# Kernel tuning notes

Hardware: AMD Instinct MI355X
Metric: run time of the kernel (lower is better)

## Reference

```python
import jax, jax.numpy as jnp
from jax import lax
import numpy as np
import math

# ---- static hyperparameters (from init_kwargs) ----
NUM_RAY = 64
NUM_RAY2 = NUM_RAY * NUM_RAY
NUM_SAMPLE = 64
STEP = 1.0 / (NUM_SAMPLE - 1)
RK = 3                       # RK4Range: neighbor cube side
K = 64                       # Num_RIGuassKernel per axis
PH = (192, 192, 192)         # PhantomSize (D, H, W)
THETA_X, THETA_Y, THETA_Z = 0.1, 0.05, 0.02
CENTER = (0.5, 0.5, 0.5)

# ---- constant neighbor offsets and kernel-center grids (Process_Parameter) ----
half = (RK - 1) // 2
_r = np.arange(-half, half + 1)
Xr_np, Yr_np, Zr_np = np.meshgrid(_r, _r, _r)
XR = jnp.asarray(Xr_np.flatten().reshape(1, RK ** 3), dtype=jnp.float32)
YR = jnp.asarray(Yr_np.flatten().reshape(1, RK ** 3), dtype=jnp.float32)
ZR = jnp.asarray(Zr_np.flatten().reshape(1, RK ** 3), dtype=jnp.float32)
_c = np.linspace(0, 1, K, dtype='float32')
Xc_np, Yc_np, Zc_np = np.meshgrid(_c, _c, _c)
XC = jnp.asarray(Xc_np.flatten())
YC = jnp.asarray(Yc_np.flatten())
ZC = jnp.asarray(Zc_np.flatten())

# ---- rotation matrices (Theta2TransMatrix) ----
def _build_transmats():
    def ry(t):
        c, s = math.cos(t), math.sin(t)
        return np.array([[1, 0, 0, 0], [0, c, -s, 0], [0, s, c, 0], [0, 0, 0, 1]], dtype=np.float64)
    def rx(t):
        c, s = math.cos(t), math.sin(t)
        return np.array([[c, 0, -s, 0], [0, 1, 0, 0], [s, 0, c, 0], [0, 0, 0, 1]], dtype=np.float64)
    def rz(t):
        c, s = math.cos(t), math.sin(t)
        return np.array([[c, -s, 0, 0], [s, c, 0, 0], [0, 0, 1, 0], [0, 0, 0, 1]], dtype=np.float64)
    RY, RY_ = ry(-THETA_Y), ry(THETA_Y)
    RX, RX_ = rx(THETA_X), rx(-THETA_X)
    RZ, RZ_ = rz(-THETA_Z), rz(THETA_Z)
    cx, cy, cz = CENTER
    S1 = np.eye(4); S1[3, :3] = [-cx, -cy, -cz]
    S2 = np.eye(4); S2[3, :3] = [cx, cy, cz]
    M_crd = S1 @ RZ @ RY @ RX @ S2
    M_drv = RX_ @ RY_ @ RZ_
    return jnp.asarray(M_crd, dtype=jnp.float32), jnp.asarray(M_drv, dtype=jnp.float32)

M_CRD, M_DRV = _build_transmats()


def _indexdist(x, y, z, RI):
    # x,y,z: [N]; RI: [K^3, 2] -> Gaussian-kernel interpolated n and spatial derivatives
    X, Y, Z = x[:, None], y[:, None], z[:, None]
    Xn = jnp.clip(jnp.round(X * K) + XR, 0.0, K - 1.0)
    Yn = jnp.clip(jnp.round(Y * K) + YR, 0.0, K - 1.0)
    Zn = jnp.clip(jnp.round(Z * K) + ZR, 0.0, K - 1.0)
    lin = (K * K * Yn + K * Xn + Zn).astype(jnp.int32)   # [N, RK^3]
    dx = XC[lin] - X
    dy = YC[lin] - Y
    dz = ZC[lin] - Z
    A = RI[lin, 0]
    sig = RI[lin, 1]
    inv_s2 = 1.0 / (sig * sig)
    ni = jnp.exp(-(dx * dx + dy * dy + dz * dz) * 0.5 * inv_s2) + 2e-7
    norm = jnp.sum(ni, axis=1)
    nu = ni * A
    nx = jnp.sum(nu * dx * inv_s2, axis=1)
    ny = jnp.sum(nu * dy * inv_s2, axis=1)
    nz = jnp.sum(nu * dz * inv_s2, axis=1)
    ndx = jnp.sum(ni * dx * inv_s2, axis=1)
    ndy = jnp.sum(ni * dy * inv_s2, axis=1)
    ndz = jnp.sum(ni * dz * inv_s2, axis=1)
    nu_s = jnp.sum(nu, axis=1)
    n = nu_s / norm
    inv_norm2 = 1.0 / (norm * norm)
    nx = (norm * nx - nu_s * ndx) * inv_norm2
    ny = (norm * ny - nu_s * ndy) * inv_norm2
    nz = (norm * nz - nu_s * ndz) * inv_norm2
    return n, nx, ny, nz


def _rayeq(z0, xy0, RI):
    ones = jnp.ones_like(z0)
    t = jnp.stack([xy0[:, 2], xy0[:, 0], z0, ones], axis=1) @ M_CRD
    n, dndx_, dndy_, dndz_ = _indexdist(t[:, 1], t[:, 0], t[:, 2], RI)
    d = jnp.stack([dndy_, dndx_, dndz_, ones], axis=1) @ M_DRV
    dndx, dndz, dndy = d[:, 1], d[:, 2], d[:, 0]
    dX1 = xy0[:, 1]
    dX2 = (dndx - dndz * dX1) * (1.0 + dX1 * dX1) / n
    dY1 = xy0[:, 3]
    dY2 = (dndy - dndz * dY1) * (1.0 + dY1 * dY1) / n
    return jnp.stack([dX1, dX2, dY1, dY2], axis=1)


def _ray_tracing(xyz0, RI):
    def step_fn(xyz, _):
        deriv = _rayeq(xyz[:, 4], xyz[:, 0:4], RI)
        xyzi = jnp.concatenate([xyz[:, 0:4] + deriv * STEP, (xyz[:, 4] + STEP)[:, None]], axis=1)
        return xyzi, xyzi
    _, rest = lax.scan(step_fn, xyz0, None, length=NUM_SAMPLE - 1)
    return jnp.concatenate([xyz0[None], rest], axis=0)   # [S, N, 5]


def _resize_axis_linear(a, axis, out_len):
    # align_corners=True 1D linear resize along `axis`
    in_len = a.shape[axis]
    pos = jnp.linspace(0.0, in_len - 1.0, out_len)
    i0 = jnp.clip(jnp.floor(pos).astype(jnp.int32), 0, in_len - 2)
    w = (pos - i0.astype(pos.dtype)).astype(a.dtype)
    a0 = jnp.take(a, i0, axis=axis)
    a1 = jnp.take(a, i0 + 1, axis=axis)
    shape = [1] * a.ndim
    shape[axis] = out_len
    w = w.reshape(shape)
    return a0 * (1.0 - w) + a1 * w


def _grid_sample_3d(vol, gx, gy, gz):
    # torch F.grid_sample trilinear, align_corners=True, padding_mode='zeros'
    D, H, W = vol.shape
    ix = (gx + 1.0) * 0.5 * (W - 1)
    iy = (gy + 1.0) * 0.5 * (H - 1)
    iz = (gz + 1.0) * 0.5 * (D - 1)
    x0 = jnp.floor(ix); y0 = jnp.floor(iy); z0 = jnp.floor(iz)
    fx = ix - x0; fy = iy - y0; fz = iz - z0
    out = jnp.zeros_like(ix)
    for dz in (0, 1):
        for dyy in (0, 1):
            for dxx in (0, 1):
                xi = x0 + dxx; yi = y0 + dyy; zi = z0 + dz
                wgt = (jnp.where(dxx == 1, fx, 1.0 - fx)
                       * jnp.where(dyy == 1, fy, 1.0 - fy)
                       * jnp.where(dz == 1, fz, 1.0 - fz))
                inb = ((xi >= 0) & (xi <= W - 1) & (yi >= 0) & (yi <= H - 1)
                       & (zi >= 0) & (zi <= D - 1))
                xc = jnp.clip(xi, 0, W - 1).astype(jnp.int32)
                yc = jnp.clip(yi, 0, H - 1).astype(jnp.int32)
                zc = jnp.clip(zi, 0, D - 1).astype(jnp.int32)
                out = out + jnp.where(inb, wgt * vol[zc, yc, xc], 0.0)
    return out


def setup_inputs() -> dict:
    key = jax.random.key(0)
    k1, k2, k3, k4, k5 = jax.random.split(key, 5)
    Phantom = jax.random.uniform(k1, (1, 1) + PH, dtype=jnp.float32)
    A = jax.random.uniform(k2, (K ** 3, 1), dtype=jnp.float32) * 0.9 + 0.1
    sig = jax.random.uniform(k3, (K ** 3, 1), dtype=jnp.float32) * 0.8 + 0.2
    RefractionIndex = jnp.concatenate([A, sig], axis=1)
    xy = jax.random.uniform(k4, (NUM_RAY2, 2), dtype=jnp.float32) * 0.8 + 0.1
    slopes = jax.random.normal(k5, (NUM_RAY2, 2), dtype=jnp.float32) * 0.05
    z0 = jnp.zeros((NUM_RAY2, 1), dtype=jnp.float32)
    # layout [x, dx/dz, y, dy/dz, z]
    RayInit = jnp.concatenate([xy[:, :1], slopes[:, :1], xy[:, 1:], slopes[:, 1:], z0], axis=1)
    return {"Phantom": Phantom, "RefractionIndex": RefractionIndex, "RayInit": RayInit}


def reference(Phantom, RefractionIndex, RayInit):
    RayInit = RayInit.reshape(NUM_RAY2, 5)
    RI = RefractionIndex.reshape(K ** 3, 2)
    paths = _ray_tracing(RayInit, RI)          # [S, N, 5]
    paths = paths * 2.0 - 1.0
    # paths -> [3, R, R, S] mesh of (x, y, z) coordinates
    mesh = jnp.stack([
        paths[:, :, 0].T.reshape(NUM_RAY, NUM_RAY, NUM_SAMPLE),
        paths[:, :, 2].T.reshape(NUM_RAY, NUM_RAY, NUM_SAMPLE),
        paths[:, :, 4].T.reshape(NUM_RAY, NUM_RAY, NUM_SAMPLE),
    ], axis=0)
    # trilinear resize (align_corners=True) to PhantomSize
    for ax, out_len in zip((1, 2, 3), PH):
        mesh = _resize_axis_linear(mesh, ax, out_len)   # [3, D, H, W]
    vol = Phantom.reshape(PH)
    out = _grid_sample_3d(vol, mesh[0], mesh[1], mesh[2])
    return out.reshape((1, 1) + PH)
```

## Files before the change

kernel.cpp:

```cpp
#include <hip/hip_runtime.h>
#include <math.h>

#define NRAY2 4096
#define NSAMP 64
#define PHD 192
#define PLANE (PHD*PHD)
constexpr float STEP = 1.0f / 63.0f;

struct Mats { float crd[16]; float drv[16]; };

static void mat_mul4(const double* A, const double* B, double* C) {
    for (int i = 0; i < 4; ++i)
        for (int j = 0; j < 4; ++j) {
            double s = 0.0;
            for (int k = 0; k < 4; ++k) s += A[i*4+k] * B[k*4+j];
            C[i*4+j] = s;
        }
}

static void build_mats(Mats& M) {
    const double tx = 0.1, ty = 0.05, tz = 0.02;
    const double cx = 0.5, cy = 0.5, cz = 0.5;
    auto ry = [](double t, double* m) {
        double c = cos(t), s = sin(t);
        double v[16] = {1,0,0,0, 0,c,-s,0, 0,s,c,0, 0,0,0,1};
        for (int i = 0; i < 16; ++i) m[i] = v[i];
    };
    auto rx = [](double t, double* m) {
        double c = cos(t), s = sin(t);
        double v[16] = {c,0,-s,0, 0,1,0,0, s,0,c,0, 0,0,0,1};
        for (int i = 0; i < 16; ++i) m[i] = v[i];
    };
    auto rz = [](double t, double* m) {
        double c = cos(t), s = sin(t);
        double v[16] = {c,-s,0,0, s,c,0,0, 0,0,1,0, 0,0,0,1};
        for (int i = 0; i < 16; ++i) m[i] = v[i];
    };
    double RY[16], RY_[16], RX[16], RX_[16], RZ[16], RZ_[16];
    ry(-ty, RY); ry(ty, RY_);
    rx(tx, RX);  rx(-tx, RX_);
    rz(-tz, RZ); rz(tz, RZ_);
    double S1[16] = {1,0,0,0, 0,1,0,0, 0,0,1,0, -cx,-cy,-cz,1};
    double S2[16] = {1,0,0,0, 0,1,0,0, 0,0,1,0,  cx, cy, cz,1};
    double t1[16], t2[16], t3[16], Mc[16], Md[16];
    mat_mul4(S1, RZ, t1);
    mat_mul4(t1, RY, t2);
    mat_mul4(t2, RX, t3);
    mat_mul4(t3, S2, Mc);
    mat_mul4(RX_, RY_, t1);
    mat_mul4(t1, RZ_, Md);
    for (int i = 0; i < 16; ++i) { M.crd[i] = (float)Mc[i]; M.drv[i] = (float)Md[i]; }
}

template<int CTRL>
__device__ __forceinline__ void dpp_level8(float* v) {
    int t[8];
    #pragma unroll
    for (int i = 0; i < 8; ++i)
        t[i] = __builtin_amdgcn_update_dpp(0, __float_as_int(v[i]), CTRL, 0xF, 0xF, true);
    #pragma unroll
    for (int i = 0; i < 8; ++i) v[i] += __int_as_float(t[i]);
}

__device__ __forceinline__ void red8_16(float* v) {
    dpp_level8<0x121>(v);
    dpp_level8<0x122>(v);
    dpp_level8<0x124>(v);
    dpp_level8<0x128>(v);
}

__global__ __launch_bounds__(64, 1) void ray_trace_kernel(
    const float* __restrict__ RI,
    const float* __restrict__ RayInit,
    float* __restrict__ meshXT,
    float* __restrict__ meshYT,
    Mats M)
{
    __shared__ float lX[NSAMP][4];
    __shared__ float lY[NSAMP][4];

    const int tid = threadIdx.x;
    const int nb  = tid & 15;
    const int rl  = tid >> 4;
    const int ray = blockIdx.x * 4 + rl;
    const bool act2 = nb < 11;

    const int n1 = nb, n2 = nb + 16;
    const float xr1 = (float)((n1/3)%3 - 1), yr1 = (float)(n1/9 - 1), zr1 = (float)(n1%3 - 1);
    const float xr2 = (float)((n2/3)%3 - 1), yr2 = (float)(n2/9 - 1), zr2 = (float)(n2%3 - 1);

    float X  = RayInit[ray*5 + 0];
    float dX = RayInit[ray*5 + 1];
    float Y  = RayInit[ray*5 + 2];
    float dY = RayInit[ray*5 + 3];
    float z  = RayInit[ray*5 + 4];

    if (nb == 0) { lX[0][rl] = X*2.0f - 1.0f; lY[0][rl] = Y*2.0f - 1.0f; }

    auto prep = [&](float pX, float pY, float pz,
                    float& ox, float& oy, float& oz,
                    float& X1, float& Y1, float& Z1,
                    float& X2, float& Y2, float& Z2,
                    float2& r1, float2& r2) {
        float x  = pY*M.crd[1] + pX*M.crd[5] + pz*M.crd[9]  + M.crd[13];
        float y  = pY*M.crd[0] + pX*M.crd[4] + pz*M.crd[8]  + M.crd[12];
        float zz = pY*M.crd[2] + pX*M.crd[6] + pz*M.crd[10] + M.crd[14];
        float rx_ = rintf(x*64.0f), ry_ = rintf(y*64.0f), rz_ = rintf(zz*64.0f);
        X1 = __builtin_amdgcn_fmed3f(rx_ + xr1, 0.0f, 63.0f);
        Y1 = __builtin_amdgcn_fmed3f(ry_ + yr1, 0.0f, 63.0f);
        Z1 = __builtin_amdgcn_fmed3f(rz_ + zr1, 0.0f, 63.0f);
        X2 = __builtin_amdgcn_fmed3f(rx_ + xr2, 0.0f, 63.0f);
        Y2 = __builtin_amdgcn_fmed3f(ry_ + yr2, 0.0f, 63.0f);
        Z2 = __builtin_amdgcn_fmed3f(rz_ + zr2, 0.0f, 63.0f);
        int l1 = (int)(Y1*4096.0f + X1*64.0f + Z1);
        int l2 = (int)(Y2*4096.0f + X2*64.0f + Z2);
        r1 = ((const float2*)RI)[l1];
        r2 = ((const float2*)RI)[l2];
        ox = x; oy = y; oz = zz;
    };

    float cx_, cy_, cz_, Xn1, Yn1, Zn1, Xn2, Yn2, Zn2;
    float2 ri1, ri2;
    prep(X, Y, z, cx_, cy_, cz_, Xn1, Yn1, Zn1, Xn2, Yn2, Zn2, ri1, ri2);

    const float C = -0.72134752044448169f;

    #pragma unroll 7
    for (int s = 1; s < NSAMP; ++s) {
        float nX = X + dX*STEP, nY = Y + dY*STEP, nz = z + STEP;
        float ncx, ncy, ncz, mX1, mY1, mZ1, mX2, mY2, mZ2;
        float2 ri1n, ri2n;
        prep(nX, nY, nz, ncx, ncy, ncz, mX1, mY1, mZ1, mX2, mY2, mZ2, ri1n, ri2n);

        float dx1 = Xn1*(1.0f/63.0f) - cx_;
        float dy1 = Yn1*(1.0f/63.0f) - cy_;
        float dz1 = Zn1*(1.0f/63.0f) - cz_;
        float is1 = __builtin_amdgcn_rcpf(ri1.y * ri1.y);
        float d21 = dx1*dx1 + dy1*dy1 + dz1*dz1;
        float e1  = __builtin_amdgcn_exp2f(d21 * is1 * C) + 2e-7f;
        float g1x = dx1*is1, g1y = dy1*is1, g1z = dz1*is1;
        float nu1 = e1 * ri1.x;

        float dx2 = Xn2*(1.0f/63.0f) - cx_;
        float dy2 = Yn2*(1.0f/63.0f) - cy_;
        float dz2 = Zn2*(1.0f/63.0f) - cz_;
        float is2 = __builtin_amdgcn_rcpf(ri2.y * ri2.y);
        float d22 = dx2*dx2 + dy2*dy2 + dz2*dz2;
        float e2  = __builtin_amdgcn_exp2f(d22 * is2 * C) + 2e-7f;
        if (!act2) e2 = 0.0f;
        float g2x = dx2*is2, g2y = dy2*is2, g2z = dz2*is2;
        float nu2 = e2 * ri2.x;

        float v[8] = { e1 + e2,
                       nu1 + nu2,
                       nu1*g1x + nu2*g2x,
                       nu1*g1y + nu2*g2y,
                       nu1*g1z + nu2*g2z,
                       e1*g1x + e2*g2x,
                       e1*g1y + e2*g2y,
                       e1*g1z + e2*g2z };
        red8_16(v);
        float ni  = v[0], nuA = v[1];
        float sx  = v[2], sy  = v[3], sz  = v[4];
        float sdx = v[5], sdy = v[6], sdz = v[7];

        float r   = __builtin_amdgcn_rcpf(ni);
        float rn  = ni * __builtin_amdgcn_rcpf(nuA);
        float in2 = r * r;
        float gx_ = (ni*sx - nuA*sdx) * in2;
        float gy_ = (ni*sy - nuA*sdy) * in2;
        float gz_ = (ni*sz - nuA*sdz) * in2;

        float dndx = gy_*M.drv[1] + gx_*M.drv[5] + gz_*M.drv[9]  + M.drv[13];
        float dndy = gy_*M.drv[0] + gx_*M.drv[4] + gz_*M.drv[8]  + M.drv[12];
        float dndz = gy_*M.drv[2] + gx_*M.drv[6] + gz_*M.drv[10] + M.drv[14];

        float dX2 = (dndx - dndz*dX) * (1.0f + dX*dX) * rn;
        float dY2 = (dndy - dndz*dY) * (1.0f + dY*dY) * rn;

        X = nX; Y = nY; z = nz;
        dX += dX2 * STEP;
        dY += dY2 * STEP;

        if (nb == 0) { lX[s][rl] = X*2.0f - 1.0f; lY[s][rl] = Y*2.0f - 1.0f; }

        cx_ = ncx; cy_ = ncy; cz_ = ncz;
        Xn1 = mX1; Yn1 = mY1; Zn1 = mZ1;
        Xn2 = mX2; Yn2 = mY2; Zn2 = mZ2;
        ri1 = ri1n; ri2 = ri2n;
    }

    __syncthreads();

    {
        const int s = tid;
        const int ray0 = blockIdx.x * 4;
        float4 vx = *(const float4*)&lX[s][0];
        float4 vy = *(const float4*)&lY[s][0];
        *(float4*)&meshXT[s*NRAY2 + ray0] = vx;
        *(float4*)&meshYT[s*NRAY2 + ray0] = vy;
    }
}

typedef _Float16 h16;
typedef _Float16 h16v4 __attribute__((ext_vector_type(4)));

__global__ __launch_bounds__(1024) void sample_kernel(
    const float* __restrict__ vol,
    const float* __restrict__ meshXT,
    const float* __restrict__ meshYT,
    h16*   __restrict__ outTh,
    float* __restrict__ outDirect,
    int transposed)
{
    __shared__ h16    plane_h[PLANE];
    __shared__ float2 slice[64*64];

    const int tid = threadIdx.x;
    const int blk = blockIdx.x;
    const int c = (blk >> 3) + 24 * (blk & 7);

    const float D = 63.0f / 191.0f;

    {
        const float4* src = (const float4*)(vol + c * PLANE);
        h16v4* dst = (h16v4*)plane_h;
        #pragma unroll
        for (int k = 0; k < (PLANE/4)/1024; ++k) {
            float4 v = src[tid + k*1024];
            h16v4 hv = {(h16)v.x, (h16)v.y, (h16)v.z, (h16)v.w};
            dst[tid + k*1024] = hv;
        }
    }

    float ps = c * D;
    int s0 = min((int)ps, 62);
    float wcs = ps - (float)s0, wc0 = 1.0f - wcs;
    {
        const float* x0 = meshXT + s0*NRAY2;
        const float* x1 = meshXT + (s0+1)*NRAY2;
        const float* y0 = meshYT + s0*NRAY2;
        const float* y1 = meshYT + (s0+1)*NRAY2;
        #pragma unroll
        for (int k = 0; k < 4096/1024; ++k) {
            int t = tid + k*1024;
            slice[t] = make_float2(x0[t]*wc0 + x1[t]*wcs,
                                   y0[t]*wc0 + y1[t]*wcs);
        }
    }
    __syncthreads();

    #pragma unroll 1
    for (int k = 0; k < PLANE/4096; ++k) {
        const int w0 = (tid + k*1024) * 4;
        const int a  = w0 / PHD;
        const int b0 = w0 - a*PHD;

        float pa = (float)a * D;
        int   i0 = min((int)pa, 62);
        float wa = pa - (float)i0;

        float pb0 = (float)b0 * D;
        int  jmin = min((int)pb0, 62);
        int  j2   = min(jmin + 2, 63);

        float2 r0c0 = slice[i0*64 + jmin];
        float2 r0c1 = slice[i0*64 + jmin + 1];
        float2 r0c2 = slice[i0*64 + j2];
        float2 r1c0 = slice[(i0+1)*64 + jmin];
        float2 r1c1 = slice[(i0+1)*64 + jmin + 1];
        float2 r1c2 = slice[(i0+1)*64 + j2];

        float c0x = r0c0.x + wa*(r1c0.x - r0c0.x);
        float c0y = r0c0.y + wa*(r1c0.y - r0c0.y);
        float c1x = r0c1.x + wa*(r1c1.x - r0c1.x);
        float c1y = r0c1.y + wa*(r1c1.y - r0c1.y);
        float c2x = r0c2.x + wa*(r1c2.x - r0c2.x);
        float c2y = r0c2.y + wa*(r1c2.y - r0c2.y);

        h16v4 res;
        #pragma unroll
        for (int m = 0; m < 4; ++m) {
            float pb = (float)(b0 + m) * D;
            int   j0 = min((int)pb, 62);
            float wb = pb - (float)j0;
            bool  hi = (j0 != jmin);

            float sax = hi ? c1x : c0x, say = hi ? c1y : c0y;
            float sbx = hi ? c2x : c1x, sby = hi ? c2y : c1y;
            float gx = sax + wb*(sbx - sax);
            float gy = say + wb*(sby - say);

            float ix = (gx + 1.0f) * 0.5f * 191.0f;
            float iy = (gy + 1.0f) * 0.5f * 191.0f;
            float x0f = floorf(ix); float fx = ix - x0f;
            float y0f = floorf(iy); float fy = iy - y0f;

            float acc = 0.0f;
            #pragma unroll
            for (int dyy = 0; dyy < 2; ++dyy) {
                #pragma unroll
                for (int dxx = 0; dxx < 2; ++dxx) {
                    float xi = x0f + (float)dxx;
                    float yi = y0f + (float)dyy;
                    bool inb = (xi >= 0.0f) && (xi <= 191.0f) &&
                               (yi >= 0.0f) && (yi <= 191.0f);
                    int xc = min(max((int)xi, 0), PHD - 1);
                    int yc = min(max((int)yi, 0), PHD - 1);
                    float w = (dxx ? fx : 1.0f - fx) * (dyy ? fy : 1.0f - fy);
                    float val = (float)plane_h[yc*PHD + xc];
                    acc += inb ? w * val : 0.0f;
                }
            }
            res[m] = (h16)acc;
        }

        if (transposed) {
            *(h16v4*)(outTh + (size_t)c*PLANE + w0) = res;
        } else {
            #pragma unroll
            for (int m = 0; m < 4; ++m)
                outDirect[(size_t)(a*PHD + b0 + m)*PHD + c] = (float)res[m];
        }
    }
}

__global__ __launch_bounds__(256) void transpose_kernel(
    const h16* __restrict__ outTh, float* __restrict__ out)
{
    __shared__ h16 t[64][66];
    const int a  = blockIdx.z;
    const int b0 = blockIdx.x * 64;
    const int c0 = blockIdx.y * 64;
    const int tx = threadIdx.x & 63;
    const int ty = threadIdx.x >> 6;

    const h16* src = outTh + (size_t)(c0 + ty) * PLANE + a*PHD + b0 + tx;
    #pragma unroll
    for (int j = 0; j < 16; ++j)
        t[ty + 4*j][tx] = src[(size_t)(4*j) * PLANE];
    __syncthreads();

    float* dst = out + (size_t)a * PLANE + (size_t)(b0 + ty) * PHD + c0 + tx;
    #pragma unroll
    for (int j = 0; j < 16; ++j)
        dst[(size_t)(4*j) * PHD] = (float)t[tx][ty + 4*j];
}

extern "C" void kernel_launch(void* const* d_in, const int* in_sizes, int n_in,
                              void* d_out, int out_size, void* d_ws, size_t ws_size,
                              hipStream_t stream)
{
    const float* Phantom = (const float*)d_in[0];
    const float* RI      = (const float*)d_in[1];
    const float* RayInit = (const float*)d_in[2];
    float* out = (float*)d_out;

    float* meshXT = (float*)d_ws;
    float* meshYT = meshXT + NRAY2 * NSAMP;
    h16*   outTh  = (h16*)(meshYT + NRAY2 * NSAMP);

    const size_t need = (size_t)(2 * NRAY2 * NSAMP) * sizeof(float)
                      + (size_t)PHD * PLANE * sizeof(h16);
    const int use_transpose = (ws_size >= need) ? 1 : 0;

    Mats M;
    build_mats(M);

    ray_trace_kernel<<<NRAY2/4, 64, 0, stream>>>(RI, RayInit, meshXT, meshYT, M);

    if (use_transpose) {
        sample_kernel<<<PHD, 1024, 0, stream>>>(Phantom, meshXT, meshYT,
                                                outTh, nullptr, 1);
        transpose_kernel<<<dim3(3, 3, PHD), 256, 0, stream>>>(outTh, out);
    } else {
        sample_kernel<<<PHD, 1024, 0, stream>>>(Phantom, meshXT, meshYT,
                                                nullptr, out, 0);
    }
}
```

Before: 140.8 us.

## Process eight rays per wavefront with four neighbors per lane

Changes the ray-trace work split so each lane handles four of the 27 neighbor kernels instead of two, and a 64-lane block traces 8 rays instead of 4. The cross-lane reduction drops from four DPP levels to three, and half as many blocks are launched. Each lane now does more serial exp/rcp work and issues more gathers per step, and the explicit unroll pragma on the sample loop was removed, which may affect latency hiding in the serial ray recurrence.

```diff
diff --git a/kernel.cpp b/kernel.cpp
--- a/kernel.cpp
+++ b/kernel.cpp
@@ -62,11 +62,10 @@
     for (int i = 0; i < 8; ++i) v[i] += __int_as_float(t[i]);
 }
 
-__device__ __forceinline__ void red8_16(float* v) {
-    dpp_level8<0x121>(v);
-    dpp_level8<0x122>(v);
-    dpp_level8<0x124>(v);
-    dpp_level8<0x128>(v);
+__device__ __forceinline__ void red8_8(float* v) {
+    dpp_level8<0xB1>(v);
+    dpp_level8<0x4E>(v);
+    dpp_level8<0x141>(v);
 }
 
 __global__ __launch_bounds__(64, 1) void ray_trace_kernel(
@@ -76,18 +75,25 @@
     float* __restrict__ meshYT,
     Mats M)
 {
-    __shared__ float lX[NSAMP][4];
-    __shared__ float lY[NSAMP][4];
+    __shared__ float lX[NSAMP][8];
+    __shared__ float lY[NSAMP][8];
 
     const int tid = threadIdx.x;
-    const int nb  = tid & 15;
-    const int rl  = tid >> 4;
-    const int ray = blockIdx.x * 4 + rl;
-    const bool act2 = nb < 11;
-
-    const int n1 = nb, n2 = nb + 16;
-    const float xr1 = (float)((n1/3)%3 - 1), yr1 = (float)(n1/9 - 1), zr1 = (float)(n1%3 - 1);
-    const float xr2 = (float)((n2/3)%3 - 1), yr2 = (float)(n2/9 - 1), zr2 = (float)(n2%3 - 1);
+    const int nb  = tid & 7;
+    const int rl  = tid >> 3;
+    const int ray = blockIdx.x * 8 + rl;
+
+    float xr[4], yr[4], zr[4];
+    bool  act[4];
+    #pragma unroll
+    for (int k = 0; k < 4; ++k) {
+        int n = nb + 8*k;
+        act[k] = (n < 27);
+        int nn = act[k] ? n : 0;
+        xr[k] = (float)((nn/3)%3 - 1);
+        yr[k] = (float)(nn/9 - 1);
+        zr[k] = (float)(nn%3 - 1);
+    }
 
     float X  = RayInit[ray*5 + 0];
     float dX = RayInit[ray*5 + 1];
@@ -98,68 +104,51 @@
     if (nb == 0) { lX[0][rl] = X*2.0f - 1.0f; lY[0][rl] = Y*2.0f - 1.0f; }
 
     auto prep = [&](float pX, float pY, float pz,
-                    float& ox, float& oy, float& oz,
-                    float& X1, float& Y1, float& Z1,
-                    float& X2, float& Y2, float& Z2,
-                    float2& r1, float2& r2) {
+                    float* dxo, float* dyo, float* dzo, float2* rio) {
         float x  = pY*M.crd[1] + pX*M.crd[5] + pz*M.crd[9]  + M.crd[13];
         float y  = pY*M.crd[0] + pX*M.crd[4] + pz*M.crd[8]  + M.crd[12];
         float zz = pY*M.crd[2] + pX*M.crd[6] + pz*M.crd[10] + M.crd[14];
         float rx_ = rintf(x*64.0f), ry_ = rintf(y*64.0f), rz_ = rintf(zz*64.0f);
-        X1 = __builtin_amdgcn_fmed3f(rx_ + xr1, 0.0f, 63.0f);
-        Y1 = __builtin_amdgcn_fmed3f(ry_ + yr1, 0.0f, 63.0f);
-        Z1 = __builtin_amdgcn_fmed3f(rz_ + zr1, 0.0f, 63.0f);
-        X2 = __builtin_amdgcn_fmed3f(rx_ + xr2, 0.0f, 63.0f);
-        Y2 = __builtin_amdgcn_fmed3f(ry_ + yr2, 0.0f, 63.0f);
-        Z2 = __builtin_amdgcn_fmed3f(rz_ + zr2, 0.0f, 63.0f);
-        int l1 = (int)(Y1*4096.0f + X1*64.0f + Z1);
-        int l2 = (int)(Y2*4096.0f + X2*64.0f + Z2);
-        r1 = ((const float2*)RI)[l1];
-        r2 = ((const float2*)RI)[l2];
-        ox = x; oy = y; oz = zz;
+        #pragma unroll
+        for (int k = 0; k < 4; ++k) {
+            float Xn = __builtin_amdgcn_fmed3f(rx_ + xr[k], 0.0f, 63.0f);
+            float Yn = __builtin_amdgcn_fmed3f(ry_ + yr[k], 0.0f, 63.0f);
+            float Zn = __builtin_amdgcn_fmed3f(rz_ + zr[k], 0.0f, 63.0f);
+            int lin = (int)(Yn*4096.0f + Xn*64.0f + Zn);
+            rio[k] = ((const float2*)RI)[lin];
+            dxo[k] = Xn*(1.0f/63.0f) - x;
+            dyo[k] = Yn*(1.0f/63.0f) - y;
+            dzo[k] = Zn*(1.0f/63.0f) - zz;
+        }
     };
 
-    float cx_, cy_, cz_, Xn1, Yn1, Zn1, Xn2, Yn2, Zn2;
-    float2 ri1, ri2;
-    prep(X, Y, z, cx_, cy_, cz_, Xn1, Yn1, Zn1, Xn2, Yn2, Zn2, ri1, ri2);
+    float dxA[4], dyA[4], dzA[4];
+    float2 riA[4];
+    prep(X, Y, z, dxA, dyA, dzA, riA);
 
     const float C = -0.72134752044448169f;
 
-    #pragma unroll 7
     for (int s = 1; s < NSAMP; ++s) {
         float nX = X + dX*STEP, nY = Y + dY*STEP, nz = z + STEP;
-        float ncx, ncy, ncz, mX1, mY1, mZ1, mX2, mY2, mZ2;
-        float2 ri1n, ri2n;
-        prep(nX, nY, nz, ncx, ncy, ncz, mX1, mY1, mZ1, mX2, mY2, mZ2, ri1n, ri2n);
-
-        float dx1 = Xn1*(1.0f/63.0f) - cx_;
-        float dy1 = Yn1*(1.0f/63.0f) - cy_;
-        float dz1 = Zn1*(1.0f/63.0f) - cz_;
-        float is1 = __builtin_amdgcn_rcpf(ri1.y * ri1.y);
-        float d21 = dx1*dx1 + dy1*dy1 + dz1*dz1;
-        float e1  = __builtin_amdgcn_exp2f(d21 * is1 * C) + 2e-7f;
-        float g1x = dx1*is1, g1y = dy1*is1, g1z = dz1*is1;
-        float nu1 = e1 * ri1.x;
-
-        float dx2 = Xn2*(1.0f/63.0f) - cx_;
-        float dy2 = Yn2*(1.0f/63.0f) - cy_;
-        float dz2 = Zn2*(1.0f/63.0f) - cz_;
-        float is2 = __builtin_amdgcn_rcpf(ri2.y * ri2.y);
-        float d22 = dx2*dx2 + dy2*dy2 + dz2*dz2;
-        float e2  = __builtin_amdgcn_exp2f(d22 * is2 * C) + 2e-7f;
-        if (!act2) e2 = 0.0f;
-        float g2x = dx2*is2, g2y = dy2*is2, g2z = dz2*is2;
-        float nu2 = e2 * ri2.x;
-
-        float v[8] = { e1 + e2,
-                       nu1 + nu2,
-                       nu1*g1x + nu2*g2x,
-                       nu1*g1y + nu2*g2y,
-                       nu1*g1z + nu2*g2z,
-                       e1*g1x + e2*g2x,
-                       e1*g1y + e2*g2y,
-                       e1*g1z + e2*g2z };
-        red8_16(v);
+        float dxB[4], dyB[4], dzB[4];
+        float2 riB[4];
+        prep(nX, nY, nz, dxB, dyB, dzB, riB);
+
+        float v[8] = {0,0,0,0,0,0,0,0};
+        #pragma unroll
+        for (int k = 0; k < 4; ++k) {
+            float is = __builtin_amdgcn_rcpf(riA[k].y * riA[k].y);
+            float d2 = dxA[k]*dxA[k] + dyA[k]*dyA[k] + dzA[k]*dzA[k];
+            float e  = __builtin_amdgcn_exp2f(d2 * is * C) + 2e-7f;
+            if (!act[k]) e = 0.0f;
+            float gx = dxA[k]*is, gy = dyA[k]*is, gz = dzA[k]*is;
+            float nu = e * riA[k].x;
+            v[0] += e;
+            v[1] += nu;
+            v[2] += nu*gx;  v[3] += nu*gy;  v[4] += nu*gz;
+            v[5] += e*gx;   v[6] += e*gy;   v[7] += e*gz;
+        }
+        red8_8(v);
         float ni  = v[0], nuA = v[1];
         float sx  = v[2], sy  = v[3], sz  = v[4];
         float sdx = v[5], sdy = v[6], sdz = v[7];
@@ -184,21 +173,22 @@
 
         if (nb == 0) { lX[s][rl] = X*2.0f - 1.0f; lY[s][rl] = Y*2.0f - 1.0f; }
 
-        cx_ = ncx; cy_ = ncy; cz_ = ncz;
-        Xn1 = mX1; Yn1 = mY1; Zn1 = mZ1;
-        Xn2 = mX2; Yn2 = mY2; Zn2 = mZ2;
-        ri1 = ri1n; ri2 = ri2n;
+        #pragma unroll
+        for (int k = 0; k < 4; ++k) {
+            dxA[k] = dxB[k]; dyA[k] = dyB[k]; dzA[k] = dzB[k];
+            riA[k] = riB[k];
+        }
     }
 
     __syncthreads();
 
     {
         const int s = tid;
-        const int ray0 = blockIdx.x * 4;
-        float4 vx = *(const float4*)&lX[s][0];
-        float4 vy = *(const float4*)&lY[s][0];
-        *(float4*)&meshXT[s*NRAY2 + ray0] = vx;
-        *(float4*)&meshYT[s*NRAY2 + ray0] = vy;
+        const int ray0 = blockIdx.x * 8;
+        *(float4*)&meshXT[s*NRAY2 + ray0]     = *(const float4*)&lX[s][0];
+        *(float4*)&meshXT[s*NRAY2 + ray0 + 4] = *(const float4*)&lX[s][4];
+        *(float4*)&meshYT[s*NRAY2 + ray0]     = *(const float4*)&lY[s][0];
+        *(float4*)&meshYT[s*NRAY2 + ray0 + 4] = *(const float4*)&lY[s][4];
     }
 }
 
@@ -367,7 +357,7 @@
     Mats M;
     build_mats(M);
 
-    ray_trace_kernel<<<NRAY2/4, 64, 0, stream>>>(RI, RayInit, meshXT, meshYT, M);
+    ray_trace_kernel<<<NRAY2/8, 64, 0, stream>>>(RI, RayInit, meshXT, meshYT, M);
 
     if (use_transpose) {
         sample_kernel<<<PHD, 1024, 0, stream>>>(Phantom, meshXT, meshYT,
```

Result: slower. 148.5 us (+5.5%).

## Remap neighbor cube to 9 lanes each loading 3 contiguous z-entries

Applied to the files above, without the earlier changes.

The ray-trace kernel now gives each of 9 lanes one (x,y) column of the 3x3x3 neighbour cube. Each lane loads three adjacent RI entries along z from a single clamped base, and clamp-duplicated entries are chosen with selects. The old layout used 16 lanes with two scattered gathers each. The goal is fewer scattered global loads, with the shared x/y distance terms computed once per lane. The loop now does three exp evaluations per lane instead of two, and the explicit unroll pragma was removed, which may change scheduling and latency hiding in the serial per-step loop.

```diff
diff --git a/kernel.cpp b/kernel.cpp
--- a/kernel.cpp
+++ b/kernel.cpp
@@ -83,11 +83,11 @@
     const int nb  = tid & 15;
     const int rl  = tid >> 4;
     const int ray = blockIdx.x * 4 + rl;
-    const bool act2 = nb < 11;
-
-    const int n1 = nb, n2 = nb + 16;
-    const float xr1 = (float)((n1/3)%3 - 1), yr1 = (float)(n1/9 - 1), zr1 = (float)(n1%3 - 1);
-    const float xr2 = (float)((n2/3)%3 - 1), yr2 = (float)(n2/9 - 1), zr2 = (float)(n2%3 - 1);
+    const bool act = nb < 9;
+
+    const int m9 = act ? nb : 0;
+    const float yo = (float)(m9/3 - 1);
+    const float xo = (float)(m9%3 - 1);
 
     float X  = RayInit[ray*5 + 0];
     float dX = RayInit[ray*5 + 1];
@@ -97,68 +97,71 @@
 
     if (nb == 0) { lX[0][rl] = X*2.0f - 1.0f; lY[0][rl] = Y*2.0f - 1.0f; }
 
-    auto prep = [&](float pX, float pY, float pz,
-                    float& ox, float& oy, float& oz,
-                    float& X1, float& Y1, float& Z1,
-                    float& X2, float& Y2, float& Z2,
-                    float2& r1, float2& r2) {
+    struct St {
+        float dx, dy;
+        float dz0, dz1, dz2;
+        float s1, s2;
+        float2 r0, r1, r2;
+    };
+
+    auto prep = [&](float pX, float pY, float pz, St& st) {
         float x  = pY*M.crd[1] + pX*M.crd[5] + pz*M.crd[9]  + M.crd[13];
         float y  = pY*M.crd[0] + pX*M.crd[4] + pz*M.crd[8]  + M.crd[12];
         float zz = pY*M.crd[2] + pX*M.crd[6] + pz*M.crd[10] + M.crd[14];
         float rx_ = rintf(x*64.0f), ry_ = rintf(y*64.0f), rz_ = rintf(zz*64.0f);
-        X1 = __builtin_amdgcn_fmed3f(rx_ + xr1, 0.0f, 63.0f);
-        Y1 = __builtin_amdgcn_fmed3f(ry_ + yr1, 0.0f, 63.0f);
-        Z1 = __builtin_amdgcn_fmed3f(rz_ + zr1, 0.0f, 63.0f);
-        X2 = __builtin_amdgcn_fmed3f(rx_ + xr2, 0.0f, 63.0f);
-        Y2 = __builtin_amdgcn_fmed3f(ry_ + yr2, 0.0f, 63.0f);
-        Z2 = __builtin_amdgcn_fmed3f(rz_ + zr2, 0.0f, 63.0f);
-        int l1 = (int)(Y1*4096.0f + X1*64.0f + Z1);
-        int l2 = (int)(Y2*4096.0f + X2*64.0f + Z2);
-        r1 = ((const float2*)RI)[l1];
-        r2 = ((const float2*)RI)[l2];
-        ox = x; oy = y; oz = zz;
-    };
-
-    float cx_, cy_, cz_, Xn1, Yn1, Zn1, Xn2, Yn2, Zn2;
-    float2 ri1, ri2;
-    prep(X, Y, z, cx_, cy_, cz_, Xn1, Yn1, Zn1, Xn2, Yn2, Zn2, ri1, ri2);
+        float Xn = __builtin_amdgcn_fmed3f(rx_ + xo, 0.0f, 63.0f);
+        float Yn = __builtin_amdgcn_fmed3f(ry_ + yo, 0.0f, 63.0f);
+        float Zb = __builtin_amdgcn_fmed3f(rz_ - 1.0f, 0.0f, 61.0f);
+        float Z0 = __builtin_amdgcn_fmed3f(rz_ - 1.0f, 0.0f, 63.0f);
+        float Z1 = __builtin_amdgcn_fmed3f(rz_,        0.0f, 63.0f);
+        float Z2 = __builtin_amdgcn_fmed3f(rz_ + 1.0f, 0.0f, 63.0f);
+        st.dx  = Xn*(1.0f/63.0f) - x;
+        st.dy  = Yn*(1.0f/63.0f) - y;
+        st.dz0 = Z0*(1.0f/63.0f) - zz;
+        st.dz1 = Z1*(1.0f/63.0f) - zz;
+        st.dz2 = Z2*(1.0f/63.0f) - zz;
+        st.s1  = Z1 - Zb;
+        st.s2  = Z2 - Zb;
+        int lin = (int)(Yn*4096.0f + Xn*64.0f + Zb);
+        const float2* p = (const float2*)RI + lin;
+        st.r0 = p[0];
+        st.r1 = p[1];
+        st.r2 = p[2];
+    };
+
+    St A;
+    prep(X, Y, z, A);
 
     const float C = -0.72134752044448169f;
 
-    #pragma unroll 7
     for (int s = 1; s < NSAMP; ++s) {
         float nX = X + dX*STEP, nY = Y + dY*STEP, nz = z + STEP;
-        float ncx, ncy, ncz, mX1, mY1, mZ1, mX2, mY2, mZ2;
-        float2 ri1n, ri2n;
-        prep(nX, nY, nz, ncx, ncy, ncz, mX1, mY1, mZ1, mX2, mY2, mZ2, ri1n, ri2n);
-
-        float dx1 = Xn1*(1.0f/63.0f) - cx_;
-        float dy1 = Yn1*(1.0f/63.0f) - cy_;
-        float dz1 = Zn1*(1.0f/63.0f) - cz_;
-        float is1 = __builtin_amdgcn_rcpf(ri1.y * ri1.y);
-        float d21 = dx1*dx1 + dy1*dy1 + dz1*dz1;
-        float e1  = __builtin_amdgcn_exp2f(d21 * is1 * C) + 2e-7f;
-        float g1x = dx1*is1, g1y = dy1*is1, g1z = dz1*is1;
-        float nu1 = e1 * ri1.x;
-
-        float dx2 = Xn2*(1.0f/63.0f) - cx_;
-        float dy2 = Yn2*(1.0f/63.0f) - cy_;
-        float dz2 = Zn2*(1.0f/63.0f) - cz_;
-        float is2 = __builtin_amdgcn_rcpf(ri2.y * ri2.y);
-        float d22 = dx2*dx2 + dy2*dy2 + dz2*dz2;
-        float e2  = __builtin_amdgcn_exp2f(d22 * is2 * C) + 2e-7f;
-        if (!act2) e2 = 0.0f;
-        float g2x = dx2*is2, g2y = dy2*is2, g2z = dz2*is2;
-        float nu2 = e2 * ri2.x;
-
-        float v[8] = { e1 + e2,
-                       nu1 + nu2,
-                       nu1*g1x + nu2*g2x,
-                       nu1*g1y + nu2*g2y,
-                       nu1*g1z + nu2*g2z,
-                       e1*g1x + e2*g2x,
-                       e1*g1y + e2*g2y,
-                       e1*g1z + e2*g2z };
+        St B;
+        prep(nX, nY, nz, B);
+
+        float2 ri0 = (A.s1 > 1.5f) ? A.r1 : A.r0;
+        float2 ri1 = (A.s1 > 1.5f) ? A.r2 :
+                     ((A.s1 > 0.5f) ? A.r1 : A.r0);
+        float2 ri2 = (A.s2 > 1.5f) ? A.r2 :
+                     ((A.s2 > 0.5f) ? A.r1 : A.r0);
+
+        float v[8] = {0,0,0,0,0,0,0,0};
+        float dzs[3] = {A.dz0, A.dz1, A.dz2};
+        float2 ris[3] = {ri0, ri1, ri2};
+        float dxy2 = A.dx*A.dx + A.dy*A.dy;
+        #pragma unroll
+        for (int k = 0; k < 3; ++k) {
+            float is = __builtin_amdgcn_rcpf(ris[k].y * ris[k].y);
+            float d2 = dxy2 + dzs[k]*dzs[k];
+            float e  = __builtin_amdgcn_exp2f(d2 * is * C) + 2e-7f;
+            if (!act) e = 0.0f;
+            float gx = A.dx*is, gy = A.dy*is, gz = dzs[k]*is;
+            float nu = e * ris[k].x;
+            v[0] += e;
+            v[1] += nu;
+            v[2] += nu*gx;  v[3] += nu*gy;  v[4] += nu*gz;
+            v[5] += e*gx;   v[6] += e*gy;   v[7] += e*gz;
+        }
         red8_16(v);
         float ni  = v[0], nuA = v[1];
         float sx  = v[2], sy  = v[3], sz  = v[4];
@@ -184,10 +187,7 @@
 
         if (nb == 0) { lX[s][rl] = X*2.0f - 1.0f; lY[s][rl] = Y*2.0f - 1.0f; }
 
-        cx_ = ncx; cy_ = ncy; cz_ = ncz;
-        Xn1 = mX1; Yn1 = mY1; Zn1 = mZ1;
-        Xn2 = mX2; Yn2 = mY2; Zn2 = mZ2;
-        ri1 = ri1n; ri2 = ri2n;
+        A = B;
     }
 
     __syncthreads();
```

Result: no change. 142.5 us (+1.2%).
